# Kernel tuning notes

Measured on AMD Instinct MI355X. Metric: run time of the kernel, lower is better.

Reference implementation:

```python
import jax, jax.numpy as jnp
import numpy as np

D_MODEL = 1024
NHEAD = 16
HEAD_DIM = D_MODEL // NHEAD  # 64
Q_STRIDE = 2
KV_STRIDE = 1
ROPE_BASE = 10000.0


def _rope_tables(positions):
    # positions: [L] int -> cos/sin [L, HEAD_DIM]
    half = HEAD_DIM // 2
    inv_freq = 1.0 / (ROPE_BASE ** (jnp.arange(half, dtype=jnp.float32) / half))
    freqs = positions.astype(jnp.float32)[:, None] * inv_freq[None, :]  # [L, half]
    emb = jnp.concatenate([freqs, freqs], axis=-1)  # [L, HEAD_DIM]
    return jnp.cos(emb), jnp.sin(emb)


def _rotate_half(x):
    half = x.shape[-1] // 2
    return jnp.concatenate([-x[..., half:], x[..., :half]], axis=-1)


def _apply_rope(x, cos, sin):
    # x: [B, H, L, D]; cos/sin: [L, D] broadcast over B, H
    return x * cos + _rotate_half(x) * sin


def setup_inputs() -> dict:
    key = jax.random.key(0)
    ks = jax.random.split(key, 10)
    B, S, K = 4, 1024, 2048
    s = 0.02
    return {
        "query": jax.random.normal(ks[0], (B, S, D_MODEL), jnp.float32),
        "kv": jax.random.normal(ks[1], (B, K, D_MODEL), jnp.float32),
        "q_w": jax.random.normal(ks[2], (D_MODEL, D_MODEL), jnp.float32) * s,
        "q_b": jax.random.normal(ks[3], (D_MODEL,), jnp.float32) * s,
        "k_w": jax.random.normal(ks[4], (D_MODEL, D_MODEL), jnp.float32) * s,
        "k_b": jax.random.normal(ks[5], (D_MODEL,), jnp.float32) * s,
        "v_w": jax.random.normal(ks[6], (D_MODEL, D_MODEL), jnp.float32) * s,
        "v_b": jax.random.normal(ks[7], (D_MODEL,), jnp.float32) * s,
        "out_w": jax.random.normal(ks[8], (D_MODEL, D_MODEL), jnp.float32) * s,
        "out_b": jax.random.normal(ks[9], (D_MODEL,), jnp.float32) * s,
    }


def reference(query, kv, q_w, q_b, k_w, k_b, v_w, v_b, out_w, out_b):
    B, S, _ = query.shape
    K = kv.shape[1]
    # Projections (torch Linear: x @ W^T + b), reshape to [B, H, L, D]
    q = (query @ q_w.T + q_b).reshape(B, S, NHEAD, HEAD_DIM).transpose(0, 2, 1, 3)
    k = (kv @ k_w.T + k_b).reshape(B, K, NHEAD, HEAD_DIM).transpose(0, 2, 1, 3)
    v = (kv @ v_w.T + v_b).reshape(B, K, NHEAD, HEAD_DIM).transpose(0, 2, 1, 3)
    # RoPE at strided original frame positions
    q_cos, q_sin = _rope_tables(jnp.arange(S) * Q_STRIDE)
    k_cos, k_sin = _rope_tables(jnp.arange(K) * KV_STRIDE)
    q = _apply_rope(q, q_cos, q_sin)
    k = _apply_rope(k, k_cos, k_sin)
    scale = 1.0 / np.sqrt(HEAD_DIM).astype(np.float32)
    attn = jnp.einsum('bhsd,bhkd->bhsk', q, k) * scale  # [B, H, S, K]
    attn = jax.nn.softmax(attn, axis=-1)
    out = jnp.einsum('bhsk,bhkd->bhsd', attn, v)
    out = out.transpose(0, 2, 1, 3).reshape(B, S, D_MODEL)
    return out @ out_w.T + out_b
```

## Files before the change

### kernel.cpp

```cpp
#include <hip/hip_runtime.h>
#include <hip/hip_bf16.h>

#define D_MODEL 1024
#define NHEAD   16
#define HD      64
#define SQ      1024
#define SK      2048

typedef __attribute__((ext_vector_type(8))) short bh8;
typedef __attribute__((ext_vector_type(4))) float fx4;

#define QSCALE 0.1803368801111204f

__device__ __forceinline__ unsigned short f2bf(float f) {
  union { float f; unsigned u; } v; v.f = f;
  return (unsigned short)((v.u + 0x7FFFu + ((v.u >> 16) & 1u)) >> 16);
}

__device__ __forceinline__ float bf2f(unsigned short u) {
  union { unsigned u; float f; } v; v.u = ((unsigned)u) << 16; return v.f;
}

#define GLOAD_LDS16(gp, lp)                                                  \
  __builtin_amdgcn_global_load_lds(                                         \
      (const __attribute__((address_space(1))) unsigned int*)(gp),          \
      (__attribute__((address_space(3))) unsigned int*)(lp), 16, 0, 0)

__global__ __launch_bounds__(256) void cvt_kernel(
    const float* __restrict__ q, const float* __restrict__ kv,
    const float* __restrict__ qw, const float* __restrict__ kw,
    const float* __restrict__ vw, const float* __restrict__ ow,
    unsigned short* __restrict__ qx, unsigned short* __restrict__ kvx,
    unsigned short* __restrict__ qwx, unsigned short* __restrict__ kwx,
    unsigned short* __restrict__ vwx, unsigned short* __restrict__ owx)
{
  const int idx = blockIdx.x * 256 + threadIdx.x;
  const float* src; unsigned short* dst; size_t off;
  if (idx < 524288)        { src = q;  dst = qx;  off = idx; }
  else if (idx < 1572864)  { src = kv; dst = kvx; off = idx - 524288; }
  else {
    const int w = idx - 1572864; const int sel = w >> 17; off = w & 131071;
    src = sel == 0 ? qw : sel == 1 ? kw : sel == 2 ? vw : ow;
    dst = sel == 0 ? qwx : sel == 1 ? kwx : sel == 2 ? vwx : owx;
  }
  const float4 a = ((const float4*)src)[off * 2];
  const float4 b = ((const float4*)src)[off * 2 + 1];
  bh8 r;
  r[0] = (short)f2bf(a.x); r[1] = (short)f2bf(a.y);
  r[2] = (short)f2bf(a.z); r[3] = (short)f2bf(a.w);
  r[4] = (short)f2bf(b.x); r[5] = (short)f2bf(b.y);
  r[6] = (short)f2bf(b.z); r[7] = (short)f2bf(b.w);
  *(bh8*)(dst + off * 8) = r;
}

template <int MODE, int MI>
__global__ __launch_bounds__(256) void proj_kernel(
    const unsigned short* __restrict__ X,
    const unsigned short* __restrict__ W0, const unsigned short* __restrict__ W1,
    const float* __restrict__ b0, const float* __restrict__ b1,
    unsigned short* __restrict__ out0, unsigned short* __restrict__ out1,
    float* __restrict__ outf)
{
  constexpr int BM = MI * 32;
  constexpr int LSH = (MODE == 1) ? 11 : 10;
  __shared__ unsigned short Alds[BM * 32];
  __shared__ unsigned short Blds[128 * 32];

  const int t = threadIdx.x;
  const int lane = t & 63, w = t >> 6;
  const int lr = lane & 15, g = lane >> 4, kl = g * 8;
  const int row0 = blockIdx.y * BM;
  const int colB = blockIdx.x * 128;
  const int wrow = (w >> 1) * (MI * 16);
  const int wcol = (w & 1) * 64;

  const unsigned short* Wsrc = W0;
  const float* bias = b0;
  unsigned short* outp = out0;
  int colW = colB;
  bool isV = false;
  if (MODE == 1 && colB >= 1024) {
    Wsrc = W1; bias = b1; outp = out1; colW = colB - 1024; isV = true;
  }

  const int srow = t >> 2, schunk = (t & 3) * 8;

  fx4 acc[MI][4] = {};
  for (int k0 = 0; k0 < 1024; k0 += 32) {
    __syncthreads();
    GLOAD_LDS16(X + (size_t)(row0 + srow) * 1024 + k0 + schunk, &Alds[t * 8]);
    if (MI == 4)
      GLOAD_LDS16(X + (size_t)(row0 + 64 + srow) * 1024 + k0 + schunk, &Alds[2048 + t * 8]);
    GLOAD_LDS16(Wsrc + (size_t)(colW + srow) * 1024 + k0 + schunk, &Blds[t * 8]);
    GLOAD_LDS16(Wsrc + (size_t)(colW + 64 + srow) * 1024 + k0 + schunk, &Blds[2048 + t * 8]);
    __syncthreads();

    bh8 af[MI], bf[4];
#pragma unroll
    for (int mi = 0; mi < MI; ++mi)
      af[mi] = *(const bh8*)&Alds[(wrow + mi * 16 + lr) * 32 + kl];
#pragma unroll
    for (int ni = 0; ni < 4; ++ni)
      bf[ni] = *(const bh8*)&Blds[(wcol + ni * 16 + lr) * 32 + kl];
    __builtin_amdgcn_s_setprio(1);
#pragma unroll
    for (int mi = 0; mi < MI; ++mi)
#pragma unroll
      for (int ni = 0; ni < 4; ++ni)
        acc[mi][ni] = __builtin_amdgcn_mfma_f32_16x16x32_bf16(af[mi], bf[ni], acc[mi][ni], 0, 0, 0);
    __builtin_amdgcn_s_setprio(0);
  }

  float bv[4];
#pragma unroll
  for (int ni = 0; ni < 4; ++ni) bv[ni] = bias[colW + wcol + ni * 16 + lr];
#pragma unroll
  for (int mi = 0; mi < MI; ++mi)
#pragma unroll
    for (int ni = 0; ni < 4; ++ni)
#pragma unroll
      for (int j = 0; j < 4; ++j) acc[mi][ni][j] += bv[ni];

  if (MODE == 0 || (MODE == 1 && !isV)) {
    const float c0 = 0.41524101186092029f;
    const float invf0 = exp2f(-(float)lr * c0);
    const float invf1 = exp2f(-(float)(16 + lr) * c0);
#pragma unroll
    for (int mi = 0; mi < MI; ++mi)
#pragma unroll
      for (int j = 0; j < 4; ++j) {
        const int rg = row0 + wrow + mi * 16 + 4 * g + j;
        const int s = rg & ((MODE == 0) ? 1023 : 2047);
        const float pos = (float)((MODE == 0) ? 2 * s : s);
#pragma unroll
        for (int ni = 0; ni < 2; ++ni) {
          float sn, cs;
          __sincosf(pos * (ni == 0 ? invf0 : invf1), &sn, &cs);
          const float x1 = acc[mi][ni][j], x2 = acc[mi][ni + 2][j];
          acc[mi][ni][j]     = x1 * cs - x2 * sn;
          acc[mi][ni + 2][j] = x2 * cs + x1 * sn;
        }
      }
  }

  const int h = (colW + wcol) >> 6;
#pragma unroll
  for (int mi = 0; mi < MI; ++mi)
#pragma unroll
    for (int j = 0; j < 4; ++j) {
      const int rg = row0 + wrow + mi * 16 + 4 * g + j;
      const int bb = rg >> LSH;
      const int s = rg & ((1 << LSH) - 1);
#pragma unroll
      for (int ni = 0; ni < 4; ++ni) {
        const int d = ni * 16 + lr;
        if (MODE == 0) {
          outp[(((size_t)(bb * 16 + h)) * SQ + s) * 64 + d] = f2bf(acc[mi][ni][j] * QSCALE);
        } else if (MODE == 1) {
          const size_t base = ((size_t)(bb * 16 + h)) * (SK * 64);
          if (!isV) {
            outp[base + (s >> 4) * 1024 + (d >> 5) * 512 + ((d >> 3) & 3) * 128 + (s & 15) * 8 + (d & 7)]
                = f2bf(acc[mi][ni][j]);
          } else {
            outp[base + (s >> 5) * 2048 + (d >> 4) * 512 + ((s >> 3) & 3) * 128 + (d & 15) * 8 + (s & 7)]
                = f2bf(acc[mi][ni][j]);
          }
        } else {
          outf[(size_t)rg * 1024 + colB + wcol + ni * 16 + lr] = acc[mi][ni][j];
        }
      }
    }
}

__global__ __launch_bounds__(256, 4) void attn_kernel(
    const unsigned short* __restrict__ Qr, const unsigned short* __restrict__ Kt,
    const unsigned short* __restrict__ Vt, unsigned short* __restrict__ O)
{
  __shared__ __align__(16) unsigned short smem[4 * 2304];
  __shared__ float llds[4][32];

  const int lane = threadIdx.x & 63;
  const int w = threadIdx.x >> 6;
  const int lr = lane & 15, g = lane >> 4, kl = g * 8;
  const int bid = blockIdx.x;
  const int swz = (bid & 7) * 256 + (bid >> 3);
  const int bh = swz >> 5;
  const int q0 = (swz & 31) * 32;
  const int b = bh >> 4, h = bh & 15;

  unsigned short* p_lds = smem + w * 2304;

  const unsigned short* Qp = Qr + (size_t)bh * SQ * HD;
  const unsigned short* Kp = Kt + (size_t)bh * SK * HD;
  const unsigned short* Vp = Vt + (size_t)bh * SK * HD;

  bh8 qf[2][2];
#pragma unroll
  for (int mi = 0; mi < 2; ++mi)
#pragma unroll
    for (int kk = 0; kk < 2; ++kk)
      qf[mi][kk] = *(const bh8*)(Qp + (size_t)(q0 + mi * 16 + lr) * 64 + kk * 32 + kl);

  bh8 ones;
#pragma unroll
  for (int i = 0; i < 8; ++i) ones[i] = (short)0x3F80;

  fx4 oacc[2][4] = {};
  fx4 lacc[2] = {};

  for (int t = 0; t < 8; ++t) {
    fx4 sacc[2][4] = {};
#pragma unroll
    for (int kk = 0; kk < 2; ++kk) {
      bh8 kf[4];
#pragma unroll
      for (int ni = 0; ni < 4; ++ni)
        kf[ni] = *(const bh8*)(Kp + (size_t)(w * 32 + t * 4 + ni) * 1024 + kk * 512 + g * 128 + lr * 8);
      __builtin_amdgcn_s_setprio(1);
#pragma unroll
      for (int mi = 0; mi < 2; ++mi)
#pragma unroll
        for (int ni = 0; ni < 4; ++ni)
          sacc[mi][ni] = __builtin_amdgcn_mfma_f32_16x16x32_bf16(qf[mi][kk], kf[ni], sacc[mi][ni], 0, 0, 0);
      __builtin_amdgcn_s_setprio(0);
    }

    asm volatile("s_waitcnt lgkmcnt(0)" ::: "memory");
    __builtin_amdgcn_sched_barrier(0);

#pragma unroll
    for (int mi = 0; mi < 2; ++mi)
#pragma unroll
      for (int ni = 0; ni < 4; ++ni) {
        float p0, p1, p2, p3;
        asm("v_exp_f32 %0, %1" : "=v"(p0) : "v"(sacc[mi][ni][0]));
        asm("v_exp_f32 %0, %1" : "=v"(p1) : "v"(sacc[mi][ni][1]));
        asm("v_exp_f32 %0, %1" : "=v"(p2) : "v"(sacc[mi][ni][2]));
        asm("v_exp_f32 %0, %1" : "=v"(p3) : "v"(sacc[mi][ni][3]));
        unsigned lo, hi;
        asm("v_cvt_pk_bf16_f32 %0, %1, %2" : "=v"(lo) : "v"(p0), "v"(p1));
        asm("v_cvt_pk_bf16_f32 %0, %1, %2" : "=v"(hi) : "v"(p2), "v"(p3));
        unsigned short* base = &p_lds[(mi * 16 + 4 * g) * 68 + ni * 16 + lr];
        base[0]   = (unsigned short)lo;
        base[68]  = (unsigned short)(lo >> 16);
        base[136] = (unsigned short)hi;
        base[204] = (unsigned short)(hi >> 16);
      }

    asm volatile("s_waitcnt lgkmcnt(0)" ::: "memory");
    __builtin_amdgcn_sched_barrier(0);

#pragma unroll
    for (int kk = 0; kk < 2; ++kk) {
      bh8 pa[2], vb[4];
#pragma unroll
      for (int mi = 0; mi < 2; ++mi) {
        const unsigned short* pp = &p_lds[(mi * 16 + lr) * 68 + kk * 32 + kl];
        const short4 a = *(const short4*)pp;
        const short4 c = *(const short4*)(pp + 4);
        pa[mi][0] = a.x; pa[mi][1] = a.y; pa[mi][2] = a.z; pa[mi][3] = a.w;
        pa[mi][4] = c.x; pa[mi][5] = c.y; pa[mi][6] = c.z; pa[mi][7] = c.w;
      }
#pragma unroll
      for (int ni = 0; ni < 4; ++ni)
        vb[ni] = *(const bh8*)(Vp + (size_t)(w * 16 + t * 2 + kk) * 2048 + ni * 512 + g * 128 + lr * 8);
      __builtin_amdgcn_s_setprio(1);
#pragma unroll
      for (int mi = 0; mi < 2; ++mi) {
#pragma unroll
        for (int ni = 0; ni < 4; ++ni)
          oacc[mi][ni] = __builtin_amdgcn_mfma_f32_16x16x32_bf16(pa[mi], vb[ni], oacc[mi][ni], 0, 0, 0);
        lacc[mi] = __builtin_amdgcn_mfma_f32_16x16x32_bf16(pa[mi], ones, lacc[mi], 0, 0, 0);
      }
      __builtin_amdgcn_s_setprio(0);
    }
  }

  if (lr == 0) {
#pragma unroll
    for (int mi = 0; mi < 2; ++mi)
#pragma unroll
      for (int j = 0; j < 4; ++j)
        llds[w][mi * 16 + 4 * g + j] = lacc[mi][j];
  }

  asm volatile("s_waitcnt lgkmcnt(0)" ::: "memory");
  __builtin_amdgcn_sched_barrier(0);
  unsigned short* opart = smem + w * 2304;
#pragma unroll
  for (int mi = 0; mi < 2; ++mi)
#pragma unroll
    for (int j = 0; j < 4; ++j) {
      const int row = mi * 16 + 4 * g + j;
#pragma unroll
      for (int ni = 0; ni < 4; ++ni)
        opart[row * 72 + ni * 16 + lr] = f2bf(oacc[mi][ni][j]);
    }
  __syncthreads();

  const int row = threadIdx.x >> 3;
  const int d0 = (threadIdx.x & 7) * 8;
  float a8[8] = {};
#pragma unroll
  for (int ww = 0; ww < 4; ++ww) {
    const bh8 v = *(const bh8*)(smem + ww * 2304 + row * 72 + d0);
#pragma unroll
    for (int i = 0; i < 8; ++i) a8[i] += bf2f((unsigned short)v[i]);
  }
  const float inv = 1.0f / (llds[0][row] + llds[1][row] + llds[2][row] + llds[3][row]);
  bh8 r;
#pragma unroll
  for (int i = 0; i < 8; ++i) r[i] = (short)f2bf(a8[i] * inv);
  *(bh8*)&O[((size_t)(b * SQ + q0 + row)) * D_MODEL + h * 64 + d0] = r;
}

extern "C" void kernel_launch(void* const* d_in, const int* in_sizes, int n_in,
                              void* d_out, int out_size, void* d_ws, size_t ws_size,
                              hipStream_t stream) {
  (void)in_sizes; (void)n_in; (void)out_size; (void)ws_size;
  const float* query = (const float*)d_in[0];
  const float* kv    = (const float*)d_in[1];
  const float* q_w   = (const float*)d_in[2];
  const float* q_b   = (const float*)d_in[3];
  const float* k_w   = (const float*)d_in[4];
  const float* k_b   = (const float*)d_in[5];
  const float* v_w   = (const float*)d_in[6];
  const float* v_b   = (const float*)d_in[7];
  const float* out_w = (const float*)d_in[8];
  const float* out_b = (const float*)d_in[9];
  float* out = (float*)d_out;

  unsigned short* ws = (unsigned short*)d_ws;
  unsigned short* qx     = ws;
  unsigned short* kvx    = ws + ((size_t)4  << 20);
  unsigned short* qwx    = ws + ((size_t)12 << 20);
  unsigned short* kwx    = ws + ((size_t)13 << 20);
  unsigned short* vwx    = ws + ((size_t)14 << 20);
  unsigned short* owx    = ws + ((size_t)15 << 20);
  unsigned short* q_rope = ws + ((size_t)16 << 20);
  unsigned short* k_t    = ws + ((size_t)20 << 20);
  unsigned short* v_t    = ws + ((size_t)28 << 20);
  unsigned short* attn_o = qx;

  hipLaunchKernelGGL(cvt_kernel, dim3(8192), dim3(256), 0, stream,
                     query, kv, q_w, k_w, v_w, out_w, qx, kvx, qwx, kwx, vwx, owx);
  hipLaunchKernelGGL((proj_kernel<0, 4>), dim3(8, 32), dim3(256), 0, stream,
                     qx, qwx, nullptr, q_b, nullptr, q_rope, nullptr, nullptr);
  hipLaunchKernelGGL((proj_kernel<1, 4>), dim3(16, 64), dim3(256), 0, stream,
                     kvx, kwx, vwx, k_b, v_b, k_t, v_t, nullptr);
  hipLaunchKernelGGL(attn_kernel, dim3(2048), dim3(256), 0, stream,
                     q_rope, k_t, v_t, attn_o);
  hipLaunchKernelGGL((proj_kernel<2, 4>), dim3(8, 32), dim3(256), 0, stream,
                     attn_o, owx, nullptr, out_b, nullptr, nullptr, nullptr, out);
}
```

Measured before the change: 177.5 us.

## Merge Q and KV projections into one launch with double-buffered LDS staging

Combines the Q projection and the K/V projection into a single 1280-block kernel, with a block-index swizzle that spreads work across XCDs. It also double-buffers the A/B LDS tiles in both projection GEMMs, so the next k-slice's global-to-LDS loads are issued before the current slice's MFMAs, dropping one barrier per iteration. The output projection becomes its own specialised kernel. The aim is to remove a launch boundary and tail, and to overlap memory loads with matrix math, at the cost of twice the LDS per block and a runtime branch between Q and K/V.

```diff
diff --git a/kernel.cpp b/kernel.cpp
--- a/kernel.cpp
+++ b/kernel.cpp
@@ -53,58 +53,67 @@
   *(bh8*)(dst + off * 8) = r;
 }
 
-template <int MODE, int MI>
-__global__ __launch_bounds__(256) void proj_kernel(
-    const unsigned short* __restrict__ X,
-    const unsigned short* __restrict__ W0, const unsigned short* __restrict__ W1,
-    const float* __restrict__ b0, const float* __restrict__ b1,
-    unsigned short* __restrict__ out0, unsigned short* __restrict__ out1,
-    float* __restrict__ outf)
+__global__ __launch_bounds__(256) void qkv_kernel(
+    const unsigned short* __restrict__ qx, const unsigned short* __restrict__ kvx,
+    const unsigned short* __restrict__ qw, const unsigned short* __restrict__ kw,
+    const unsigned short* __restrict__ vw,
+    const float* __restrict__ qb, const float* __restrict__ kb,
+    const float* __restrict__ vb,
+    unsigned short* __restrict__ outq, unsigned short* __restrict__ outk,
+    unsigned short* __restrict__ outv)
 {
-  constexpr int BM = MI * 32;
-  constexpr int LSH = (MODE == 1) ? 11 : 10;
-  __shared__ unsigned short Alds[BM * 32];
-  __shared__ unsigned short Blds[128 * 32];
+  __shared__ unsigned short Alds[2][4096];
+  __shared__ unsigned short Blds[2][4096];
 
   const int t = threadIdx.x;
   const int lane = t & 63, w = t >> 6;
   const int lr = lane & 15, g = lane >> 4, kl = g * 8;
-  const int row0 = blockIdx.y * BM;
-  const int colB = blockIdx.x * 128;
-  const int wrow = (w >> 1) * (MI * 16);
+  const int bid = (blockIdx.x & 7) * 160 + (blockIdx.x >> 3);
+  const bool isQ = bid >= 1024;
+  int bx, by;
+  if (isQ) { const int tq = bid - 1024; bx = tq >> 5; by = tq & 31; }
+  else     { bx = bid >> 6; by = bid & 63; }
+  const int row0 = by * 128;
+  const int colB = bx * 128;
+  const int wrow = (w >> 1) * 64;
   const int wcol = (w & 1) * 64;
 
-  const unsigned short* Wsrc = W0;
-  const float* bias = b0;
-  unsigned short* outp = out0;
-  int colW = colB;
-  bool isV = false;
-  if (MODE == 1 && colB >= 1024) {
-    Wsrc = W1; bias = b1; outp = out1; colW = colB - 1024; isV = true;
-  }
+  const unsigned short* X = isQ ? qx : kvx;
+  const unsigned short* Wsrc; const float* bias; int colW; bool isK = false;
+  if (isQ)              { Wsrc = qw; bias = qb; colW = colB; }
+  else if (colB < 1024) { Wsrc = kw; bias = kb; colW = colB; isK = true; }
+  else                  { Wsrc = vw; bias = vb; colW = colB - 1024; }
 
   const int srow = t >> 2, schunk = (t & 3) * 8;
 
-  fx4 acc[MI][4] = {};
+#define STAGE_P(k0_, bi_) do {                                                        \
+    GLOAD_LDS16(X + (size_t)(row0 + srow) * 1024 + (k0_) + schunk,                    \
+                &Alds[bi_][t * 8]);                                                   \
+    GLOAD_LDS16(X + (size_t)(row0 + 64 + srow) * 1024 + (k0_) + schunk,               \
+                &Alds[bi_][2048 + t * 8]);                                            \
+    GLOAD_LDS16(Wsrc + (size_t)(colW + srow) * 1024 + (k0_) + schunk,                 \
+                &Blds[bi_][t * 8]);                                                   \
+    GLOAD_LDS16(Wsrc + (size_t)(colW + 64 + srow) * 1024 + (k0_) + schunk,            \
+                &Blds[bi_][2048 + t * 8]);                                            \
+  } while (0)
+
+  fx4 acc[4][4] = {};
+  STAGE_P(0, 0);
   for (int k0 = 0; k0 < 1024; k0 += 32) {
+    const int cur = (k0 >> 5) & 1;
     __syncthreads();
-    GLOAD_LDS16(X + (size_t)(row0 + srow) * 1024 + k0 + schunk, &Alds[t * 8]);
-    if (MI == 4)
-      GLOAD_LDS16(X + (size_t)(row0 + 64 + srow) * 1024 + k0 + schunk, &Alds[2048 + t * 8]);
-    GLOAD_LDS16(Wsrc + (size_t)(colW + srow) * 1024 + k0 + schunk, &Blds[t * 8]);
-    GLOAD_LDS16(Wsrc + (size_t)(colW + 64 + srow) * 1024 + k0 + schunk, &Blds[2048 + t * 8]);
-    __syncthreads();
-
-    bh8 af[MI], bf[4];
-#pragma unroll
-    for (int mi = 0; mi < MI; ++mi)
-      af[mi] = *(const bh8*)&Alds[(wrow + mi * 16 + lr) * 32 + kl];
+    if (k0 + 32 < 1024) STAGE_P(k0 + 32, cur ^ 1);
+
+    bh8 af[4], bf[4];
+#pragma unroll
+    for (int mi = 0; mi < 4; ++mi)
+      af[mi] = *(const bh8*)&Alds[cur][(wrow + mi * 16 + lr) * 32 + kl];
 #pragma unroll
     for (int ni = 0; ni < 4; ++ni)
-      bf[ni] = *(const bh8*)&Blds[(wcol + ni * 16 + lr) * 32 + kl];
+      bf[ni] = *(const bh8*)&Blds[cur][(wcol + ni * 16 + lr) * 32 + kl];
     __builtin_amdgcn_s_setprio(1);
 #pragma unroll
-    for (int mi = 0; mi < MI; ++mi)
+    for (int mi = 0; mi < 4; ++mi)
 #pragma unroll
       for (int ni = 0; ni < 4; ++ni)
         acc[mi][ni] = __builtin_amdgcn_mfma_f32_16x16x32_bf16(af[mi], bf[ni], acc[mi][ni], 0, 0, 0);
@@ -115,23 +124,24 @@
 #pragma unroll
   for (int ni = 0; ni < 4; ++ni) bv[ni] = bias[colW + wcol + ni * 16 + lr];
 #pragma unroll
-  for (int mi = 0; mi < MI; ++mi)
+  for (int mi = 0; mi < 4; ++mi)
 #pragma unroll
     for (int ni = 0; ni < 4; ++ni)
 #pragma unroll
       for (int j = 0; j < 4; ++j) acc[mi][ni][j] += bv[ni];
 
-  if (MODE == 0 || (MODE == 1 && !isV)) {
+  const int LMASK = isQ ? 1023 : 2047;
+  if (isQ || isK) {
     const float c0 = 0.41524101186092029f;
     const float invf0 = exp2f(-(float)lr * c0);
     const float invf1 = exp2f(-(float)(16 + lr) * c0);
 #pragma unroll
-    for (int mi = 0; mi < MI; ++mi)
+    for (int mi = 0; mi < 4; ++mi)
 #pragma unroll
       for (int j = 0; j < 4; ++j) {
         const int rg = row0 + wrow + mi * 16 + 4 * g + j;
-        const int s = rg & ((MODE == 0) ? 1023 : 2047);
-        const float pos = (float)((MODE == 0) ? 2 * s : s);
+        const int s = rg & LMASK;
+        const float pos = (float)(isQ ? 2 * s : s);
 #pragma unroll
         for (int ni = 0; ni < 2; ++ni) {
           float sn, cs;
@@ -145,30 +155,91 @@
 
   const int h = (colW + wcol) >> 6;
 #pragma unroll
-  for (int mi = 0; mi < MI; ++mi)
+  for (int mi = 0; mi < 4; ++mi)
 #pragma unroll
     for (int j = 0; j < 4; ++j) {
       const int rg = row0 + wrow + mi * 16 + 4 * g + j;
-      const int bb = rg >> LSH;
-      const int s = rg & ((1 << LSH) - 1);
+      const int bb = isQ ? (rg >> 10) : (rg >> 11);
+      const int s = rg & LMASK;
 #pragma unroll
       for (int ni = 0; ni < 4; ++ni) {
         const int d = ni * 16 + lr;
-        if (MODE == 0) {
-          outp[(((size_t)(bb * 16 + h)) * SQ + s) * 64 + d] = f2bf(acc[mi][ni][j] * QSCALE);
-        } else if (MODE == 1) {
+        if (isQ) {
+          outq[(((size_t)(bb * 16 + h)) * SQ + s) * 64 + d] = f2bf(acc[mi][ni][j] * QSCALE);
+        } else {
           const size_t base = ((size_t)(bb * 16 + h)) * (SK * 64);
-          if (!isV) {
-            outp[base + (s >> 4) * 1024 + (d >> 5) * 512 + ((d >> 3) & 3) * 128 + (s & 15) * 8 + (d & 7)]
+          if (isK)
+            outk[base + (s >> 4) * 1024 + (d >> 5) * 512 + ((d >> 3) & 3) * 128 + (s & 15) * 8 + (d & 7)]
                 = f2bf(acc[mi][ni][j]);
-          } else {
-            outp[base + (s >> 5) * 2048 + (d >> 4) * 512 + ((s >> 3) & 3) * 128 + (d & 15) * 8 + (s & 7)]
+          else
+            outv[base + (s >> 5) * 2048 + (d >> 4) * 512 + ((s >> 3) & 3) * 128 + (d & 15) * 8 + (s & 7)]
                 = f2bf(acc[mi][ni][j]);
-          }
-        } else {
-          outf[(size_t)rg * 1024 + colB + wcol + ni * 16 + lr] = acc[mi][ni][j];
         }
       }
+    }
+}
+
+__global__ __launch_bounds__(256) void oproj_kernel(
+    const unsigned short* __restrict__ A, const unsigned short* __restrict__ W,
+    const float* __restrict__ bias, float* __restrict__ out)
+{
+  __shared__ unsigned short Alds[2][4096];
+  __shared__ unsigned short Blds[2][4096];
+
+  const int t = threadIdx.x;
+  const int lane = t & 63, w = t >> 6;
+  const int lr = lane & 15, g = lane >> 4, kl = g * 8;
+  const int row0 = blockIdx.y * 128;
+  const int colB = blockIdx.x * 128;
+  const int wrow = (w >> 1) * 64;
+  const int wcol = (w & 1) * 64;
+  const int srow = t >> 2, schunk = (t & 3) * 8;
+
+#define STAGE_O(k0_, bi_) do {                                                        \
+    GLOAD_LDS16(A + (size_t)(row0 + srow) * 1024 + (k0_) + schunk,                    \
+                &Alds[bi_][t * 8]);                                                   \
+    GLOAD_LDS16(A + (size_t)(row0 + 64 + srow) * 1024 + (k0_) + schunk,               \
+                &Alds[bi_][2048 + t * 8]);                                            \
+    GLOAD_LDS16(W + (size_t)(colB + srow) * 1024 + (k0_) + schunk,                    \
+                &Blds[bi_][t * 8]);                                                   \
+    GLOAD_LDS16(W + (size_t)(colB + 64 + srow) * 1024 + (k0_) + schunk,               \
+                &Blds[bi_][2048 + t * 8]);                                            \
+  } while (0)
+
+  fx4 acc[4][4] = {};
+  STAGE_O(0, 0);
+  for (int k0 = 0; k0 < 1024; k0 += 32) {
+    const int cur = (k0 >> 5) & 1;
+    __syncthreads();
+    if (k0 + 32 < 1024) STAGE_O(k0 + 32, cur ^ 1);
+
+    bh8 af[4], bf[4];
+#pragma unroll
+    for (int mi = 0; mi < 4; ++mi)
+      af[mi] = *(const bh8*)&Alds[cur][(wrow + mi * 16 + lr) * 32 + kl];
+#pragma unroll
+    for (int ni = 0; ni < 4; ++ni)
+      bf[ni] = *(const bh8*)&Blds[cur][(wcol + ni * 16 + lr) * 32 + kl];
+    __builtin_amdgcn_s_setprio(1);
+#pragma unroll
+    for (int mi = 0; mi < 4; ++mi)
+#pragma unroll
+      for (int ni = 0; ni < 4; ++ni)
+        acc[mi][ni] = __builtin_amdgcn_mfma_f32_16x16x32_bf16(af[mi], bf[ni], acc[mi][ni], 0, 0, 0);
+    __builtin_amdgcn_s_setprio(0);
+  }
+
+  float bv[4];
+#pragma unroll
+  for (int ni = 0; ni < 4; ++ni) bv[ni] = bias[colB + wcol + ni * 16 + lr];
+#pragma unroll
+  for (int mi = 0; mi < 4; ++mi)
+#pragma unroll
+    for (int j = 0; j < 4; ++j) {
+      const int rg = row0 + wrow + mi * 16 + 4 * g + j;
+#pragma unroll
+      for (int ni = 0; ni < 4; ++ni)
+        out[(size_t)rg * 1024 + colB + wcol + ni * 16 + lr] = acc[mi][ni][j] + bv[ni];
     }
 }
 
@@ -344,12 +415,10 @@
 
   hipLaunchKernelGGL(cvt_kernel, dim3(8192), dim3(256), 0, stream,
                      query, kv, q_w, k_w, v_w, out_w, qx, kvx, qwx, kwx, vwx, owx);
-  hipLaunchKernelGGL((proj_kernel<0, 4>), dim3(8, 32), dim3(256), 0, stream,
-                     qx, qwx, nullptr, q_b, nullptr, q_rope, nullptr, nullptr);
-  hipLaunchKernelGGL((proj_kernel<1, 4>), dim3(16, 64), dim3(256), 0, stream,
-                     kvx, kwx, vwx, k_b, v_b, k_t, v_t, nullptr);
+  hipLaunchKernelGGL(qkv_kernel, dim3(1280), dim3(256), 0, stream,
+                     qx, kvx, qwx, kwx, vwx, q_b, k_b, v_b, q_rope, k_t, v_t);
   hipLaunchKernelGGL(attn_kernel, dim3(2048), dim3(256), 0, stream,
                      q_rope, k_t, v_t, attn_o);
-  hipLaunchKernelGGL((proj_kernel<2, 4>), dim3(8, 32), dim3(256), 0, stream,
-                     attn_o, owx, nullptr, out_b, nullptr, nullptr, nullptr, out);
-}
+  hipLaunchKernelGGL(oproj_kernel, dim3(8, 32), dim3(256), 0, stream,
+                     attn_o, owx, out_b, out);
+}
```

New measurement: 172.5 us. 1.03x faster.
